# Kernel tuning notes

Measured on AMD Instinct MI355X. Metric: run time of the kernel, lower is better.

## Reference

```python
import jax, jax.numpy as jnp
import numpy as np

D = 1024       # embedding_dim
H = 16         # num_attention_heads
B = 2
S = 2048       # seq_len == context_len


def setup_inputs() -> dict:
    key = jax.random.key(0)
    k1, k2, k3 = jax.random.split(key, 3)
    X = jax.random.normal(k1, (B, S, D), dtype=jnp.float32)
    W_qkv = jax.random.normal(k2, (D, 3 * D), dtype=jnp.float32) * 0.02
    b_qkv = jnp.zeros((3 * D,), dtype=jnp.float32)
    W_out = jax.random.normal(k3, (D, D), dtype=jnp.float32) * 0.02
    b_out = jnp.zeros((D,), dtype=jnp.float32)
    return {"X": X, "W_qkv": W_qkv, "b_qkv": b_qkv, "W_out": W_out, "b_out": b_out}


def reference(X, W_qkv, b_qkv, W_out, b_out):
    b, s, d = X.shape
    hd = d // H
    # fused QKV projection (GPT-2 Conv1D == x @ W + b)
    qkv = X @ W_qkv + b_qkv                       # [b, s, 3d]
    q, k, v = jnp.split(qkv, 3, axis=2)
    # [b, h, s, hd]
    q = q.reshape(b, s, H, hd).transpose(0, 2, 1, 3)
    k = k.reshape(b, s, H, hd).transpose(0, 2, 1, 3)
    v = v.reshape(b, s, H, hd).transpose(0, 2, 1, 3)
    # NOTE: source scales by rsqrt(embedding_dim), not head_dim
    scale = 1.0 / jnp.sqrt(jnp.float32(d))
    scores = jnp.einsum("bhqd,bhkd->bhqk", q, k) * scale
    causal = jnp.tril(jnp.ones((s, s), dtype=bool))
    scores = jnp.where(causal[None, None], scores, -jnp.inf)
    # attention_dropout applied pre-softmax in source; identity at eval (p used here = 0)
    probs = jax.nn.softmax(scores, axis=-1)
    attn = jnp.einsum("bhqk,bhkd->bhqd", probs, v)
    attn = attn.transpose(0, 2, 1, 3).reshape(b, s, d)
    out = attn @ W_out + b_out                    # outwards proj; dropout eval = identity
    return out
```

## Files before the change

kernel.cpp:

```cpp
#include <hip/hip_runtime.h>

#define S_LEN 2048
#define DIM   1024
#define NHEAD 16
#define HDIM  64
#define Q_PRESCALE 0.045084220027780106f

typedef __attribute__((ext_vector_type(8))) short  short8;
typedef __attribute__((ext_vector_type(4))) float  floatx4;
typedef __attribute__((ext_vector_type(4))) unsigned short ushort4v;
typedef __attribute__((ext_vector_type(4))) unsigned int uintx4;

__device__ inline unsigned short f2bf(float f) {
  unsigned v = __builtin_bit_cast(unsigned, f);
  v += 0x7FFFu + ((v >> 16) & 1u);
  return (unsigned short)(v >> 16);
}

__device__ inline unsigned cvt_pk_bf16(float a, float b) {
  unsigned r;
  asm("v_cvt_pk_bf16_f32 %0, %1, %2" : "=v"(r) : "v"(a), "v"(b));
  return r;
}

__device__ inline void permlane16_swap_rw(unsigned &a, unsigned &b) {
  asm("v_permlane16_swap_b32 %0, %1" : "+v"(a), "+v"(b));
}

__device__ inline void async16(const unsigned short* g, unsigned short* l) {
  __builtin_amdgcn_global_load_lds(
      (const __attribute__((address_space(1))) unsigned int*)g,
      (__attribute__((address_space(3))) unsigned int*)l, 16, 0, 0);
}

__global__ __launch_bounds__(256) void prep_kernel(
    const float* __restrict__ X, const float* __restrict__ Wqkv,
    const float* __restrict__ Wout, unsigned short* __restrict__ Xb,
    unsigned short* __restrict__ Wqkvt, unsigned short* __restrict__ Woutt) {
  const int j = blockIdx.x, t = threadIdx.x;
  if (j >= 4096) {
    int i = ((j - 4096) * 256 + t) * 8;
    float4 a = *(const float4*)&X[i];
    float4 b = *(const float4*)&X[i + 4];
    short8 o;
    o[0] = (short)f2bf(a.x); o[1] = (short)f2bf(a.y);
    o[2] = (short)f2bf(a.z); o[3] = (short)f2bf(a.w);
    o[4] = (short)f2bf(b.x); o[5] = (short)f2bf(b.y);
    o[6] = (short)f2bf(b.z); o[7] = (short)f2bf(b.w);
    *(short8*)&Xb[i] = o;
    return;
  }
  __shared__ unsigned short tile[32][33];
  const float* in; unsigned short* out; int N, tn, tk;
  if (j < 3072) { in = Wqkv; out = Wqkvt; N = 3072; tn = j % 96; tk = j / 96; }
  else { int u = j - 3072; in = Wout; out = Woutt; N = 1024; tn = u & 31; tk = u >> 5; }
  const int n0 = tn * 32, k0 = tk * 32;
  const int tx = t & 31, ty = t >> 5;
#pragma unroll
  for (int i = 0; i < 32; i += 8)
    tile[ty + i][tx] = f2bf(in[(size_t)(k0 + ty + i) * N + n0 + tx]);
  __syncthreads();
#pragma unroll
  for (int i = 0; i < 32; i += 8)
    out[(size_t)(n0 + ty + i) * 1024 + k0 + tx] = tile[tx][ty + i];
}

#define GEMM128_BODY(APTR, BPTR)                                                   \
  __shared__ __align__(16) unsigned short As[128][64];                             \
  __shared__ __align__(16) unsigned short Bs[128][64];                             \
  const int m0 = blockIdx.y * 128, n0 = blockIdx.x * 128;                          \
  const int t = threadIdx.x, lane = t & 63, wave = t >> 6;                         \
  const int quad = lane >> 4, l16 = lane & 15;                                     \
  const int wm = (wave >> 1) * 64, wn = (wave & 1) * 64;                           \
  const int lr = lane >> 3, lc = lane & 7, sc8 = (lc ^ lr) * 8;                    \
  const int sw = l16 & 7;                                                          \
  const int pA0 = (quad ^ sw) * 8, pA1 = ((4 + quad) ^ sw) * 8;                    \
  floatx4 acc[4][4];                                                               \
  _Pragma("unroll") for (int mi = 0; mi < 4; mi++)                                 \
      _Pragma("unroll") for (int ni = 0; ni < 4; ni++)                             \
          acc[mi][ni] = (floatx4){0.f, 0.f, 0.f, 0.f};                             \
  for (int k0 = 0; k0 < DIM; k0 += 64) {                                           \
    _Pragma("unroll") for (int i = 0; i < 4; i++) {                                \
      int rb = wave * 32 + i * 8;                                                  \
      async16(&APTR[(size_t)(m0 + rb + lr) * DIM + k0 + sc8], &As[rb][0]);         \
      async16(&BPTR[(size_t)(n0 + rb + lr) * DIM + k0 + sc8], &Bs[rb][0]);         \
    }                                                                              \
    __syncthreads();                                                               \
    short8 a0[4], a1[4];                                                           \
    _Pragma("unroll") for (int mi = 0; mi < 4; mi++) {                             \
      int row = wm + mi * 16 + l16;                                                \
      a0[mi] = *(const short8*)&As[row][pA0];                                      \
      a1[mi] = *(const short8*)&As[row][pA1];                                      \
    }                                                                              \
    _Pragma("unroll") for (int ni = 0; ni < 4; ni++) {                             \
      int row = wn + ni * 16 + l16;                                                \
      short8 b0 = *(const short8*)&Bs[row][pA0];                                   \
      short8 b1 = *(const short8*)&Bs[row][pA1];                                   \
      _Pragma("unroll") for (int mi = 0; mi < 4; mi++) {                           \
        acc[mi][ni] = __builtin_amdgcn_mfma_f32_16x16x32_bf16(a0[mi], b0, acc[mi][ni], 0, 0, 0); \
        acc[mi][ni] = __builtin_amdgcn_mfma_f32_16x16x32_bf16(a1[mi], b1, acc[mi][ni], 0, 0, 0); \
      }                                                                            \
    }                                                                              \
    __syncthreads();                                                               \
  }

__global__ __launch_bounds__(256) void gemm_qkv128(
    const unsigned short* __restrict__ Xb,
    const unsigned short* __restrict__ Wt,
    const float* __restrict__ bias,
    unsigned short* __restrict__ Qgt,
    unsigned short* __restrict__ Kg,
    unsigned short* __restrict__ Vgt) {
  GEMM128_BODY(Xb, Wt)
  const int section = n0 >> 10;
  const int head = ((n0 + wn) >> 6) & 15;
#pragma unroll
  for (int mi = 0; mi < 4; mi++) {
    int mg = m0 + wm + mi * 16 + quad * 4;
    int bb = mg >> 11, sb = mg & 2047;
    size_t y = (size_t)bb * NHEAD + head;
    if (section == 2) {
#pragma unroll
      for (int ni = 0; ni < 4; ni++) {
        int hdi = ni * 16 + l16;
        float bv = bias[n0 + wn + hdi];
        ushort4v o;
#pragma unroll
        for (int r = 0; r < 4; r++) o[r] = f2bf(acc[mi][ni][r] + bv);
        *(ushort4v*)&Vgt[(y * HDIM + hdi) * S_LEN + sb] = o;
      }
    } else if (section == 0) {
#pragma unroll
      for (int ni = 0; ni < 4; ni++) {
        int hdi = ni * 16 + l16;
        float bv = bias[n0 + wn + hdi];
        ushort4v o;
#pragma unroll
        for (int r = 0; r < 4; r++) o[r] = f2bf((acc[mi][ni][r] + bv) * Q_PRESCALE);
        *(ushort4v*)&Qgt[(y * HDIM + hdi) * S_LEN + sb] = o;
      }
    } else {
#pragma unroll
      for (int ni = 0; ni < 4; ni++) {
        int hdi = ni * 16 + l16;
        float bv = bias[n0 + wn + hdi];
#pragma unroll
        for (int r = 0; r < 4; r++)
          Kg[(y * S_LEN + sb + r) * HDIM + hdi] = f2bf(acc[mi][ni][r] + bv);
      }
    }
  }
}

__global__ __launch_bounds__(128) void gemm_out64(
    const unsigned short* __restrict__ A,
    const unsigned short* __restrict__ Wt,
    const float* __restrict__ bias,
    float* __restrict__ outp) {
  __shared__ __align__(16) unsigned short As[64][64];
  __shared__ __align__(16) unsigned short Bs[64][64];
  const int m0 = blockIdx.y * 64, n0 = blockIdx.x * 64;
  const int t = threadIdx.x, lane = t & 63, wave = t >> 6;
  const int quad = lane >> 4, l16 = lane & 15;
  const int wn = wave * 32;
  const int lr = lane >> 3, lc = lane & 7, sc8 = (lc ^ lr) * 8;
  const int sw = l16 & 7;
  const int pA0 = (quad ^ sw) * 8, pA1 = ((4 + quad) ^ sw) * 8;
  floatx4 acc[4][2];
#pragma unroll
  for (int mi = 0; mi < 4; mi++)
#pragma unroll
    for (int ni = 0; ni < 2; ni++) acc[mi][ni] = (floatx4){0.f, 0.f, 0.f, 0.f};

  for (int k0 = 0; k0 < DIM; k0 += 64) {
#pragma unroll
    for (int i = 0; i < 4; i++) {
      int rb = wave * 32 + i * 8;
      async16(&A[(size_t)(m0 + rb + lr) * DIM + k0 + sc8], &As[rb][0]);
      async16(&Wt[(size_t)(n0 + rb + lr) * DIM + k0 + sc8], &Bs[rb][0]);
    }
    __syncthreads();
    short8 a0[4], a1[4];
#pragma unroll
    for (int mi = 0; mi < 4; mi++) {
      int row = mi * 16 + l16;
      a0[mi] = *(const short8*)&As[row][pA0];
      a1[mi] = *(const short8*)&As[row][pA1];
    }
#pragma unroll
    for (int ni = 0; ni < 2; ni++) {
      int row = wn + ni * 16 + l16;
      short8 b0 = *(const short8*)&Bs[row][pA0];
      short8 b1 = *(const short8*)&Bs[row][pA1];
#pragma unroll
      for (int mi = 0; mi < 4; mi++) {
        acc[mi][ni] = __builtin_amdgcn_mfma_f32_16x16x32_bf16(a0[mi], b0, acc[mi][ni], 0, 0, 0);
        acc[mi][ni] = __builtin_amdgcn_mfma_f32_16x16x32_bf16(a1[mi], b1, acc[mi][ni], 0, 0, 0);
      }
    }
    __syncthreads();
  }
#pragma unroll
  for (int ni = 0; ni < 2; ni++) {
    int n = n0 + wn + ni * 16 + l16;
    float bv = bias[n];
#pragma unroll
    for (int mi = 0; mi < 4; mi++) {
      int mg = m0 + mi * 16 + quad * 4;
#pragma unroll
      for (int r = 0; r < 4; r++)
        outp[(size_t)(mg + r) * DIM + n] = acc[mi][ni][r] + bv;
    }
  }
}

__global__ __launch_bounds__(256) void gemm_qkv_kernel(
    const float* __restrict__ X,
    const unsigned short* __restrict__ Wt,
    const float* __restrict__ bias,
    unsigned short* __restrict__ Qgt,
    unsigned short* __restrict__ Kg,
    unsigned short* __restrict__ Vgt,
    int g0, int G) {
  __shared__ __align__(16) unsigned short As[64][72];
  __shared__ __align__(16) unsigned short Bs[64][72];
  const int tn = blockIdx.x;
  const int section = tn / G, within = tn % G;
  const int n0 = section * 1024 + (g0 + within) * 64;
  const int m0 = blockIdx.y * 64;
  const int t = threadIdx.x, lane = t & 63, wave = t >> 6;
  const int quad = lane >> 4, l16 = lane & 15;

  floatx4 acc[4];
#pragma unroll
  for (int i = 0; i < 4; i++) acc[i] = (floatx4){0.f, 0.f, 0.f, 0.f};

  for (int k0 = 0; k0 < DIM; k0 += 64) {
#pragma unroll
    for (int i = 0; i < 2; i++) {
      int v = t + i * 256;
      int row = v >> 3, cc = (v & 7) * 8;
      float4 f0 = *(const float4*)&X[(size_t)(m0 + row) * DIM + k0 + cc];
      float4 f1 = *(const float4*)&X[(size_t)(m0 + row) * DIM + k0 + cc + 4];
      short8 o;
      o[0] = (short)f2bf(f0.x); o[1] = (short)f2bf(f0.y);
      o[2] = (short)f2bf(f0.z); o[3] = (short)f2bf(f0.w);
      o[4] = (short)f2bf(f1.x); o[5] = (short)f2bf(f1.y);
      o[6] = (short)f2bf(f1.z); o[7] = (short)f2bf(f1.w);
      *(short8*)&As[row][cc] = o;
      *(short8*)&Bs[row][cc] = *(const short8*)&Wt[(size_t)(n0 + row) * DIM + k0 + cc];
    }
    __syncthreads();
    short8 a0 = *(const short8*)&As[wave * 16 + l16][quad * 8];
    short8 a1 = *(const short8*)&As[wave * 16 + l16][32 + quad * 8];
#pragma unroll
    for (int nt = 0; nt < 4; nt++) {
      short8 b0 = *(const short8*)&Bs[nt * 16 + l16][quad * 8];
      short8 b1 = *(const short8*)&Bs[nt * 16 + l16][32 + quad * 8];
      acc[nt] = __builtin_amdgcn_mfma_f32_16x16x32_bf16(a0, b0, acc[nt], 0, 0, 0);
      acc[nt] = __builtin_amdgcn_mfma_f32_16x16x32_bf16(a1, b1, acc[nt], 0, 0, 0);
    }
    __syncthreads();
  }

  const int mbase = m0 + wave * 16 + quad * 4;
  const int b = mbase >> 11, sbase = mbase & 2047;
  const int y = b * G + within;
  if (section == 2) {
#pragma unroll
    for (int nt = 0; nt < 4; nt++) {
      int hdi = nt * 16 + l16;
      float bv = bias[n0 + hdi];
      ushort4v o;
#pragma unroll
      for (int r = 0; r < 4; r++) o[r] = f2bf(acc[nt][r] + bv);
      *(ushort4v*)&Vgt[((size_t)y * HDIM + hdi) * S_LEN + sbase] = o;
    }
  } else if (section == 0) {
#pragma unroll
    for (int nt = 0; nt < 4; nt++) {
      int hdi = nt * 16 + l16;
      float bv = bias[n0 + hdi];
      ushort4v o;
#pragma unroll
      for (int r = 0; r < 4; r++) o[r] = f2bf((acc[nt][r] + bv) * Q_PRESCALE);
      *(ushort4v*)&Qgt[((size_t)y * HDIM + hdi) * S_LEN + sbase] = o;
    }
  } else {
#pragma unroll
    for (int nt = 0; nt < 4; nt++) {
      int hdi = nt * 16 + l16;
      float bv = bias[n0 + hdi];
#pragma unroll
      for (int r = 0; r < 4; r++)
        Kg[((size_t)y * S_LEN + sbase + r) * HDIM + hdi] = f2bf(acc[nt][r] + bv);
    }
  }
}

__global__ __launch_bounds__(256) void attn_kernel(
    const unsigned short* __restrict__ Qgt,
    const unsigned short* __restrict__ Kg,
    const unsigned short* __restrict__ Vgt,
    unsigned short* __restrict__ attnB) {
  __shared__ __align__(16) unsigned short Ks[2][64][64];
  __shared__ __align__(16) unsigned short Vs[3][64][64];

  const int y = blockIdx.x;
  const int b = y >> 4, h = y & 15;
  const int qt = 31 - blockIdx.y;
  const int q0 = qt * 64;
  const int nT = qt + 1;
  const int t = threadIdx.x;
  const int lane = t & 63, wave = t >> 6;
  const int quad = lane >> 4, l16 = lane & 15;
  const int lr = lane >> 3, lc = lane & 7;
  const int sc8 = (lc ^ lr) * 8;
  const int sw = l16 & 7;
  const int p0 = (quad ^ sw) * 8, p1 = ((4 + quad) ^ sw) * 8;

  const unsigned short* Qh = Qgt + (size_t)y * S_LEN * HDIM;
  const unsigned short* Kh = Kg + (size_t)y * S_LEN * HDIM;
  const unsigned short* Vh = Vgt + (size_t)y * HDIM * S_LEN;

  const unsigned ov = (l16 == 0) ? 0x3F803F80u : 0u;
  const uintx4 ou = {ov, ov, ov, ov};
  const short8 ones = __builtin_bit_cast(short8, ou);

  short8 aq0, aq1;
  {
    const int s = q0 + wave * 16 + l16;
#pragma unroll
    for (int j = 0; j < 8; j++) {
      aq0[j] = (short)Qh[(size_t)(quad * 8 + j) * S_LEN + s];
      aq1[j] = (short)Qh[(size_t)(32 + quad * 8 + j) * S_LEN + s];
    }
  }

  floatx4 o_acc[5];
#pragma unroll
  for (int dt = 0; dt < 5; dt++) o_acc[dt] = (floatx4){0.f, 0.f, 0.f, 0.f};

  {
    int rb = wave * 16;
#pragma unroll
    for (int i = 0; i < 2; i++) {
      async16(&Kh[(size_t)(rb + i * 8 + lr) * HDIM + sc8], &Ks[0][rb + i * 8][0]);
      async16(&Vh[(size_t)(rb + i * 8 + lr) * S_LEN + sc8], &Vs[0][rb + i * 8][0]);
    }
  }

  int prevV = 2, curV = 0, nextV = 1;
  short8 apP0, apP1;

  for (int tt = 0; tt < nT; tt++) {
    const int j0 = tt * 64;
    const int kb = tt & 1;
    __syncthreads();
    if (tt + 1 < nT) {
      int j1 = j0 + 64;
      int rb = wave * 16;
#pragma unroll
      for (int i = 0; i < 2; i++) {
        async16(&Kh[(size_t)(j1 + rb + i * 8 + lr) * HDIM + sc8], &Ks[kb ^ 1][rb + i * 8][0]);
        async16(&Vh[(size_t)(rb + i * 8 + lr) * S_LEN + j1 + sc8], &Vs[nextV][rb + i * 8][0]);
      }
    }

    floatx4 sc[4];
#pragma unroll
    for (int nt = 0; nt < 4; nt++) {
      short8 kb0 = *(const short8*)&Ks[kb][nt * 16 + l16][p0];
      short8 kb1 = *(const short8*)&Ks[kb][nt * 16 + l16][p1];
      sc[nt] = (floatx4){0.f, 0.f, 0.f, 0.f};
      sc[nt] = __builtin_amdgcn_mfma_f32_16x16x32_bf16(kb0, aq0, sc[nt], 0, 0, 0);
      sc[nt] = __builtin_amdgcn_mfma_f32_16x16x32_bf16(kb1, aq1, sc[nt], 0, 0, 0);
    }

    if (tt > 0) {
#pragma unroll
      for (int dt = 0; dt < 5; dt++) {
        short8 vb0 = (dt < 4) ? *(const short8*)&Vs[prevV][dt * 16 + l16][p0] : ones;
        short8 vb1 = (dt < 4) ? *(const short8*)&Vs[prevV][dt * 16 + l16][p1] : ones;
        o_acc[dt] = __builtin_amdgcn_mfma_f32_16x16x32_bf16(apP0, vb0, o_acc[dt], 0, 0, 0);
        o_acc[dt] = __builtin_amdgcn_mfma_f32_16x16x32_bf16(apP1, vb1, o_acc[dt], 0, 0, 0);
      }
    }

    float p[4][4];
#pragma unroll
    for (int nt = 0; nt < 4; nt++)
#pragma unroll
      for (int r = 0; r < 4; r++)
        p[nt][r] = exp2f(sc[nt][r]);
    if (j0 == q0) {
      const int ql = wave * 16 + l16;
#pragma unroll
      for (int nt = 0; nt < 4; nt++)
#pragma unroll
        for (int r = 0; r < 4; r++)
          if (nt * 16 + quad * 4 + r > ql) p[nt][r] = 0.f;
    }

    unsigned pk00 = cvt_pk_bf16(p[0][0], p[0][1]), pk01 = cvt_pk_bf16(p[0][2], p[0][3]);
    unsigned pk10 = cvt_pk_bf16(p[1][0], p[1][1]), pk11 = cvt_pk_bf16(p[1][2], p[1][3]);
    unsigned pk20 = cvt_pk_bf16(p[2][0], p[2][1]), pk21 = cvt_pk_bf16(p[2][2], p[2][3]);
    unsigned pk30 = cvt_pk_bf16(p[3][0], p[3][1]), pk31 = cvt_pk_bf16(p[3][2], p[3][3]);

    auto sa0 = __builtin_amdgcn_permlane32_swap(pk00, pk10, false, false);
    auto sa1 = __builtin_amdgcn_permlane32_swap(pk01, pk11, false, false);
    auto sb0 = __builtin_amdgcn_permlane32_swap(pk20, pk30, false, false);
    auto sb1 = __builtin_amdgcn_permlane32_swap(pk21, pk31, false, false);
    unsigned xa0 = (unsigned)sa0[0], ya0 = (unsigned)sa0[1];
    unsigned xa1 = (unsigned)sa1[0], ya1 = (unsigned)sa1[1];
    unsigned xb0 = (unsigned)sb0[0], yb0 = (unsigned)sb0[1];
    unsigned xb1 = (unsigned)sb1[0], yb1 = (unsigned)sb1[1];
    permlane16_swap_rw(xa0, ya0);
    permlane16_swap_rw(xa1, ya1);
    permlane16_swap_rw(xb0, yb0);
    permlane16_swap_rw(xb1, yb1);
    uintx4 u0 = {xa0, xa1, ya0, ya1};
    apP0 = __builtin_bit_cast(short8, u0);
    uintx4 u1 = {xb0, xb1, yb0, yb1};
    apP1 = __builtin_bit_cast(short8, u1);

    int tmp = prevV; prevV = curV; curV = nextV; nextV = tmp;
  }

#pragma unroll
  for (int dt = 0; dt < 5; dt++) {
    short8 vb0 = (dt < 4) ? *(const short8*)&Vs[prevV][dt * 16 + l16][p0] : ones;
    short8 vb1 = (dt < 4) ? *(const short8*)&Vs[prevV][dt * 16 + l16][p1] : ones;
    o_acc[dt] = __builtin_amdgcn_mfma_f32_16x16x32_bf16(apP0, vb0, o_acc[dt], 0, 0, 0);
    o_acc[dt] = __builtin_amdgcn_mfma_f32_16x16x32_bf16(apP1, vb1, o_acc[dt], 0, 0, 0);
  }

  float linv[4];
#pragma unroll
  for (int r = 0; r < 4; r++)
    linv[r] = 1.0f / __shfl(o_acc[4][r], quad << 4);
#pragma unroll
  for (int dt = 0; dt < 4; dt++)
#pragma unroll
    for (int r = 0; r < 4; r++) {
      int qg = q0 + wave * 16 + quad * 4 + r;
      attnB[(size_t)(b * S_LEN + qg) * DIM + h * HDIM + dt * 16 + l16] =
          f2bf(o_acc[dt][r] * linv[r]);
    }
}

extern "C" void kernel_launch(void* const* d_in, const int* in_sizes, int n_in,
                              void* d_out, int out_size, void* d_ws, size_t ws_size,
                              hipStream_t stream) {
  const float* X    = (const float*)d_in[0];
  const float* Wqkv = (const float*)d_in[1];
  const float* bqkv = (const float*)d_in[2];
  const float* Wout = (const float*)d_in[3];
  const float* bout = (const float*)d_in[4];
  float* outp = (float*)d_out;

  unsigned short* Wqkvt = (unsigned short*)d_ws;
  unsigned short* Woutt = Wqkvt + (size_t)3145728;
  unsigned short* attnB = Woutt + (size_t)1048576;
  unsigned short* Qgt   = attnB + (size_t)4194304;
  unsigned short* Kg    = Qgt + (size_t)4194304;
  unsigned short* Vgt   = Kg + (size_t)4194304;
  unsigned short* Xb    = Vgt + (size_t)4194304;

  const bool bigWs = ws_size >= (size_t)48 * 1024 * 1024;

  if (bigWs) {
    prep_kernel<<<6144, 256, 0, stream>>>(X, Wqkv, Wout, Xb, Wqkvt, Woutt);
    gemm_qkv128<<<dim3(24, 32), 256, 0, stream>>>(Xb, Wqkvt, bqkv, Qgt, Kg, Vgt);
  } else {
    prep_kernel<<<4096, 256, 0, stream>>>(X, Wqkv, Wout, nullptr, Wqkvt, Woutt);
    gemm_qkv_kernel<<<dim3(48, 64), 256, 0, stream>>>(
        X, Wqkvt, bqkv, Qgt, Kg, Vgt, 0, 16);
  }
  attn_kernel<<<dim3(32, 32), 256, 0, stream>>>(Qgt, Kg, Vgt, attnB);
  gemm_out64<<<dim3(16, 64), 128, 0, stream>>>(attnB, Woutt, bout, outp);
}
```

Baseline: 179.8 us.

## Double-buffer LDS tiles in QKV and output projection GEMMs

Both projection GEMMs now keep two LDS buffers for A and B. The next K-tile is fetched asynchronously while MFMAs run on the current one, and the separate barrier after each load is removed. The aim is to hide global-to-LDS load latency behind matrix compute. In exchange, shared memory per block doubles (64 KB for the 128-tile kernel), which may lower occupancy.

```diff
diff --git a/kernel.cpp b/kernel.cpp
--- a/kernel.cpp
+++ b/kernel.cpp
@@ -66,8 +66,8 @@
 }
 
 #define GEMM128_BODY(APTR, BPTR)                                                   \
-  __shared__ __align__(16) unsigned short As[128][64];                             \
-  __shared__ __align__(16) unsigned short Bs[128][64];                             \
+  __shared__ __align__(16) unsigned short As[2][128][64];                          \
+  __shared__ __align__(16) unsigned short Bs[2][128][64];                          \
   const int m0 = blockIdx.y * 128, n0 = blockIdx.x * 128;                          \
   const int t = threadIdx.x, lane = t & 63, wave = t >> 6;                         \
   const int quad = lane >> 4, l16 = lane & 15;                                     \
@@ -79,23 +79,32 @@
   _Pragma("unroll") for (int mi = 0; mi < 4; mi++)                                 \
       _Pragma("unroll") for (int ni = 0; ni < 4; ni++)                             \
           acc[mi][ni] = (floatx4){0.f, 0.f, 0.f, 0.f};                             \
-  for (int k0 = 0; k0 < DIM; k0 += 64) {                                           \
-    _Pragma("unroll") for (int i = 0; i < 4; i++) {                                \
-      int rb = wave * 32 + i * 8;                                                  \
-      async16(&APTR[(size_t)(m0 + rb + lr) * DIM + k0 + sc8], &As[rb][0]);         \
-      async16(&BPTR[(size_t)(n0 + rb + lr) * DIM + k0 + sc8], &Bs[rb][0]);         \
+  _Pragma("unroll") for (int i = 0; i < 4; i++) {                                  \
+    int rb = wave * 32 + i * 8;                                                    \
+    async16(&APTR[(size_t)(m0 + rb + lr) * DIM + sc8], &As[0][rb][0]);             \
+    async16(&BPTR[(size_t)(n0 + rb + lr) * DIM + sc8], &Bs[0][rb][0]);             \
+  }                                                                                \
+  __syncthreads();                                                                 \
+  for (int kt = 0; kt < DIM / 64; ++kt) {                                          \
+    const int cur = kt & 1;                                                        \
+    if (kt + 1 < DIM / 64) {                                                       \
+      const int k1 = (kt + 1) * 64;                                                \
+      _Pragma("unroll") for (int i = 0; i < 4; i++) {                              \
+        int rb = wave * 32 + i * 8;                                                \
+        async16(&APTR[(size_t)(m0 + rb + lr) * DIM + k1 + sc8], &As[cur ^ 1][rb][0]); \
+        async16(&BPTR[(size_t)(n0 + rb + lr) * DIM + k1 + sc8], &Bs[cur ^ 1][rb][0]); \
+      }                                                                            \
     }                                                                              \
-    __syncthreads();                                                               \
     short8 a0[4], a1[4];                                                           \
     _Pragma("unroll") for (int mi = 0; mi < 4; mi++) {                             \
       int row = wm + mi * 16 + l16;                                                \
-      a0[mi] = *(const short8*)&As[row][pA0];                                      \
-      a1[mi] = *(const short8*)&As[row][pA1];                                      \
+      a0[mi] = *(const short8*)&As[cur][row][pA0];                                 \
+      a1[mi] = *(const short8*)&As[cur][row][pA1];                                 \
     }                                                                              \
     _Pragma("unroll") for (int ni = 0; ni < 4; ni++) {                             \
       int row = wn + ni * 16 + l16;                                                \
-      short8 b0 = *(const short8*)&Bs[row][pA0];                                   \
-      short8 b1 = *(const short8*)&Bs[row][pA1];                                   \
+      short8 b0 = *(const short8*)&Bs[cur][row][pA0];                              \
+      short8 b1 = *(const short8*)&Bs[cur][row][pA1];                              \
       _Pragma("unroll") for (int mi = 0; mi < 4; mi++) {                           \
         acc[mi][ni] = __builtin_amdgcn_mfma_f32_16x16x32_bf16(a0[mi], b0, acc[mi][ni], 0, 0, 0); \
         acc[mi][ni] = __builtin_amdgcn_mfma_f32_16x16x32_bf16(a1[mi], b1, acc[mi][ni], 0, 0, 0); \
@@ -157,8 +166,8 @@
     const unsigned short* __restrict__ Wt,
     const float* __restrict__ bias,
     float* __restrict__ outp) {
-  __shared__ __align__(16) unsigned short As[64][64];
-  __shared__ __align__(16) unsigned short Bs[64][64];
+  __shared__ __align__(16) unsigned short As[2][64][64];
+  __shared__ __align__(16) unsigned short Bs[2][64][64];
   const int m0 = blockIdx.y * 64, n0 = blockIdx.x * 64;
   const int t = threadIdx.x, lane = t & 63, wave = t >> 6;
   const int quad = lane >> 4, l16 = lane & 15;
@@ -172,26 +181,36 @@
 #pragma unroll
     for (int ni = 0; ni < 2; ni++) acc[mi][ni] = (floatx4){0.f, 0.f, 0.f, 0.f};
 
-  for (int k0 = 0; k0 < DIM; k0 += 64) {
-#pragma unroll
-    for (int i = 0; i < 4; i++) {
-      int rb = wave * 32 + i * 8;
-      async16(&A[(size_t)(m0 + rb + lr) * DIM + k0 + sc8], &As[rb][0]);
-      async16(&Wt[(size_t)(n0 + rb + lr) * DIM + k0 + sc8], &Bs[rb][0]);
-    }
-    __syncthreads();
+#pragma unroll
+  for (int i = 0; i < 4; i++) {
+    int rb = wave * 32 + i * 8;
+    async16(&A[(size_t)(m0 + rb + lr) * DIM + sc8], &As[0][rb][0]);
+    async16(&Wt[(size_t)(n0 + rb + lr) * DIM + sc8], &Bs[0][rb][0]);
+  }
+  __syncthreads();
+  for (int kt = 0; kt < DIM / 64; ++kt) {
+    const int cur = kt & 1;
+    if (kt + 1 < DIM / 64) {
+      const int k1 = (kt + 1) * 64;
+#pragma unroll
+      for (int i = 0; i < 4; i++) {
+        int rb = wave * 32 + i * 8;
+        async16(&A[(size_t)(m0 + rb + lr) * DIM + k1 + sc8], &As[cur ^ 1][rb][0]);
+        async16(&Wt[(size_t)(n0 + rb + lr) * DIM + k1 + sc8], &Bs[cur ^ 1][rb][0]);
+      }
+    }
     short8 a0[4], a1[4];
 #pragma unroll
     for (int mi = 0; mi < 4; mi++) {
       int row = mi * 16 + l16;
-      a0[mi] = *(const short8*)&As[row][pA0];
-      a1[mi] = *(const short8*)&As[row][pA1];
+      a0[mi] = *(const short8*)&As[cur][row][pA0];
+      a1[mi] = *(const short8*)&As[cur][row][pA1];
     }
 #pragma unroll
     for (int ni = 0; ni < 2; ni++) {
       int row = wn + ni * 16 + l16;
-      short8 b0 = *(const short8*)&Bs[row][pA0];
-      short8 b1 = *(const short8*)&Bs[row][pA1];
+      short8 b0 = *(const short8*)&Bs[cur][row][pA0];
+      short8 b1 = *(const short8*)&Bs[cur][row][pA1];
 #pragma unroll
       for (int mi = 0; mi < 4; mi++) {
         acc[mi][ni] = __builtin_amdgcn_mfma_f32_16x16x32_bf16(a0[mi], b0, acc[mi][ni], 0, 0, 0);
```

Measured after the change: 179.8 us (median of 2 runs). No clear change (-0.0%).

## Fuse X fp32-to-bf16 conversion into QKV GEMM and double-buffer LDS

Applied to the files above, without the earlier changes.

Drops the separate pass that converted X to a bf16 workspace buffer. The QKV GEMM now loads fp32 X directly, converts it in registers and stores it into LDS. The GEMM also gains double-buffered A/B tiles, so loads for the next k-tile overlap the MFMA work on the current one. This saves a full write and reread of X in bf16, at the cost of more global read traffic per tile (fp32, re-read by each of the 24 column blocks), synchronous A loads through registers, and twice the LDS use, which may lower occupancy.

```diff
diff --git a/kernel.cpp b/kernel.cpp
--- a/kernel.cpp
+++ b/kernel.cpp
@@ -34,22 +34,9 @@
 }
 
 __global__ __launch_bounds__(256) void prep_kernel(
-    const float* __restrict__ X, const float* __restrict__ Wqkv,
-    const float* __restrict__ Wout, unsigned short* __restrict__ Xb,
+    const float* __restrict__ Wqkv, const float* __restrict__ Wout,
     unsigned short* __restrict__ Wqkvt, unsigned short* __restrict__ Woutt) {
   const int j = blockIdx.x, t = threadIdx.x;
-  if (j >= 4096) {
-    int i = ((j - 4096) * 256 + t) * 8;
-    float4 a = *(const float4*)&X[i];
-    float4 b = *(const float4*)&X[i + 4];
-    short8 o;
-    o[0] = (short)f2bf(a.x); o[1] = (short)f2bf(a.y);
-    o[2] = (short)f2bf(a.z); o[3] = (short)f2bf(a.w);
-    o[4] = (short)f2bf(b.x); o[5] = (short)f2bf(b.y);
-    o[6] = (short)f2bf(b.z); o[7] = (short)f2bf(b.w);
-    *(short8*)&Xb[i] = o;
-    return;
-  }
   __shared__ unsigned short tile[32][33];
   const float* in; unsigned short* out; int N, tn, tk;
   if (j < 3072) { in = Wqkv; out = Wqkvt; N = 3072; tn = j % 96; tk = j / 96; }
@@ -65,53 +52,83 @@
     out[(size_t)(n0 + ty + i) * 1024 + k0 + tx] = tile[tx][ty + i];
 }
 
-#define GEMM128_BODY(APTR, BPTR)                                                   \
-  __shared__ __align__(16) unsigned short As[128][64];                             \
-  __shared__ __align__(16) unsigned short Bs[128][64];                             \
-  const int m0 = blockIdx.y * 128, n0 = blockIdx.x * 128;                          \
-  const int t = threadIdx.x, lane = t & 63, wave = t >> 6;                         \
-  const int quad = lane >> 4, l16 = lane & 15;                                     \
-  const int wm = (wave >> 1) * 64, wn = (wave & 1) * 64;                           \
-  const int lr = lane >> 3, lc = lane & 7, sc8 = (lc ^ lr) * 8;                    \
-  const int sw = l16 & 7;                                                          \
-  const int pA0 = (quad ^ sw) * 8, pA1 = ((4 + quad) ^ sw) * 8;                    \
-  floatx4 acc[4][4];                                                               \
-  _Pragma("unroll") for (int mi = 0; mi < 4; mi++)                                 \
-      _Pragma("unroll") for (int ni = 0; ni < 4; ni++)                             \
-          acc[mi][ni] = (floatx4){0.f, 0.f, 0.f, 0.f};                             \
-  for (int k0 = 0; k0 < DIM; k0 += 64) {                                           \
-    _Pragma("unroll") for (int i = 0; i < 4; i++) {                                \
-      int rb = wave * 32 + i * 8;                                                  \
-      async16(&APTR[(size_t)(m0 + rb + lr) * DIM + k0 + sc8], &As[rb][0]);         \
-      async16(&BPTR[(size_t)(n0 + rb + lr) * DIM + k0 + sc8], &Bs[rb][0]);         \
-    }                                                                              \
-    __syncthreads();                                                               \
-    short8 a0[4], a1[4];                                                           \
-    _Pragma("unroll") for (int mi = 0; mi < 4; mi++) {                             \
-      int row = wm + mi * 16 + l16;                                                \
-      a0[mi] = *(const short8*)&As[row][pA0];                                      \
-      a1[mi] = *(const short8*)&As[row][pA1];                                      \
-    }                                                                              \
-    _Pragma("unroll") for (int ni = 0; ni < 4; ni++) {                             \
-      int row = wn + ni * 16 + l16;                                                \
-      short8 b0 = *(const short8*)&Bs[row][pA0];                                   \
-      short8 b1 = *(const short8*)&Bs[row][pA1];                                   \
-      _Pragma("unroll") for (int mi = 0; mi < 4; mi++) {                           \
-        acc[mi][ni] = __builtin_amdgcn_mfma_f32_16x16x32_bf16(a0[mi], b0, acc[mi][ni], 0, 0, 0); \
-        acc[mi][ni] = __builtin_amdgcn_mfma_f32_16x16x32_bf16(a1[mi], b1, acc[mi][ni], 0, 0, 0); \
-      }                                                                            \
-    }                                                                              \
-    __syncthreads();                                                               \
-  }
-
 __global__ __launch_bounds__(256) void gemm_qkv128(
-    const unsigned short* __restrict__ Xb,
+    const float* __restrict__ X,
     const unsigned short* __restrict__ Wt,
     const float* __restrict__ bias,
     unsigned short* __restrict__ Qgt,
     unsigned short* __restrict__ Kg,
     unsigned short* __restrict__ Vgt) {
-  GEMM128_BODY(Xb, Wt)
+  __shared__ __align__(16) unsigned short As[2][128][64];
+  __shared__ __align__(16) unsigned short Bs[2][128][64];
+  const int m0 = blockIdx.y * 128, n0 = blockIdx.x * 128;
+  const int t = threadIdx.x, lane = t & 63, wave = t >> 6;
+  const int quad = lane >> 4, l16 = lane & 15;
+  const int wm = (wave >> 1) * 64, wn = (wave & 1) * 64;
+  const int lr = lane >> 3, lc = lane & 7, sc8 = (lc ^ lr) * 8;
+  const int sw = l16 & 7;
+  const int pA0 = (quad ^ sw) * 8, pA1 = ((4 + quad) ^ sw) * 8;
+  floatx4 acc[4][4];
+#pragma unroll
+  for (int mi = 0; mi < 4; mi++)
+#pragma unroll
+    for (int ni = 0; ni < 4; ni++) acc[mi][ni] = (floatx4){0.f, 0.f, 0.f, 0.f};
+
+#define STAGE_A_QKV(BUF, KOFF)                                                  \
+  _Pragma("unroll") for (int i = 0; i < 4; i++) {                               \
+    int rb = wave * 32 + i * 8;                                                 \
+    const float* xp = &X[(size_t)(m0 + rb + lr) * DIM + (KOFF) + sc8];          \
+    float4 f0 = *(const float4*)xp;                                             \
+    float4 f1 = *(const float4*)(xp + 4);                                       \
+    short8 o;                                                                   \
+    o[0] = (short)f2bf(f0.x); o[1] = (short)f2bf(f0.y);                         \
+    o[2] = (short)f2bf(f0.z); o[3] = (short)f2bf(f0.w);                         \
+    o[4] = (short)f2bf(f1.x); o[5] = (short)f2bf(f1.y);                         \
+    o[6] = (short)f2bf(f1.z); o[7] = (short)f2bf(f1.w);                         \
+    *(short8*)&As[BUF][rb + lr][lc * 8] = o;                                    \
+  }
+
+  STAGE_A_QKV(0, 0)
+#pragma unroll
+  for (int i = 0; i < 4; i++) {
+    int rb = wave * 32 + i * 8;
+    async16(&Wt[(size_t)(n0 + rb + lr) * DIM + sc8], &Bs[0][rb][0]);
+  }
+  __syncthreads();
+
+  for (int kt = 0; kt < DIM / 64; ++kt) {
+    const int cur = kt & 1;
+    if (kt + 1 < DIM / 64) {
+      const int k1 = (kt + 1) * 64;
+      STAGE_A_QKV(cur ^ 1, k1)
+#pragma unroll
+      for (int i = 0; i < 4; i++) {
+        int rb = wave * 32 + i * 8;
+        async16(&Wt[(size_t)(n0 + rb + lr) * DIM + k1 + sc8], &Bs[cur ^ 1][rb][0]);
+      }
+    }
+    short8 a0[4], a1[4];
+#pragma unroll
+    for (int mi = 0; mi < 4; mi++) {
+      int row = wm + mi * 16 + l16;
+      a0[mi] = *(const short8*)&As[cur][row][pA0];
+      a1[mi] = *(const short8*)&As[cur][row][pA1];
+    }
+#pragma unroll
+    for (int ni = 0; ni < 4; ni++) {
+      int row = wn + ni * 16 + l16;
+      short8 b0 = *(const short8*)&Bs[cur][row][pA0];
+      short8 b1 = *(const short8*)&Bs[cur][row][pA1];
+#pragma unroll
+      for (int mi = 0; mi < 4; mi++) {
+        acc[mi][ni] = __builtin_amdgcn_mfma_f32_16x16x32_bf16(a0[mi], b0, acc[mi][ni], 0, 0, 0);
+        acc[mi][ni] = __builtin_amdgcn_mfma_f32_16x16x32_bf16(a1[mi], b1, acc[mi][ni], 0, 0, 0);
+      }
+    }
+    __syncthreads();
+  }
+#undef STAGE_A_QKV
+
   const int section = n0 >> 10;
   const int head = ((n0 + wn) >> 6) & 15;
 #pragma unroll
@@ -465,15 +482,11 @@
   unsigned short* Qgt   = attnB + (size_t)4194304;
   unsigned short* Kg    = Qgt + (size_t)4194304;
   unsigned short* Vgt   = Kg + (size_t)4194304;
-  unsigned short* Xb    = Vgt + (size_t)4194304;
-
-  const bool bigWs = ws_size >= (size_t)48 * 1024 * 1024;
-
-  if (bigWs) {
-    prep_kernel<<<6144, 256, 0, stream>>>(X, Wqkv, Wout, Xb, Wqkvt, Woutt);
-    gemm_qkv128<<<dim3(24, 32), 256, 0, stream>>>(Xb, Wqkvt, bqkv, Qgt, Kg, Vgt);
+
+  prep_kernel<<<4096, 256, 0, stream>>>(Wqkv, Wout, Wqkvt, Woutt);
+  if (ws_size >= (size_t)41 * 1024 * 1024) {
+    gemm_qkv128<<<dim3(24, 32), 256, 0, stream>>>(X, Wqkvt, bqkv, Qgt, Kg, Vgt);
   } else {
-    prep_kernel<<<4096, 256, 0, stream>>>(X, Wqkv, Wout, nullptr, Wqkvt, Woutt);
     gemm_qkv_kernel<<<dim3(48, 64), 256, 0, stream>>>(
         X, Wqkvt, bqkv, Qgt, Kg, Vgt, 0, 16);
   }
```

Result: slower. 192.7 us (+7.1%).
